# Kernel optimization log

Measured on AMD Instinct MI355X. Metric: run time of the kernel, lower is better.

Reference implementation:

```python
import jax, jax.numpy as jnp
import numpy as np

N, E, F, H = 20000, 320000, 128, 256   # nodes, edges, in-features, hidden
M, NQ = 4096, 2048                      # lsq rows, QP variables
LAMB_MAX = 2.0


def setup_inputs() -> dict:
    key = jax.random.key(0)
    ks = jax.random.split(key, 12)
    x = jax.random.normal(ks[0], (N, F), jnp.float32)
    edge_index = jax.random.randint(ks[1], (2, E), 0, N)
    A = jax.random.normal(ks[2], (M, NQ), jnp.float32) * 0.05
    b = jax.random.normal(ks[3], (M, 1), jnp.float32)
    feat_ids = jax.random.randint(ks[4], (NQ,), 0, N)
    x_prior = jax.random.uniform(ks[5], (NQ, 1), jnp.float32)
    lamb = jnp.ones((1,), jnp.float32)
    # ChebConv K=2 weights: one linear per Chebyshev order, plus bias
    W10 = jax.random.normal(ks[6], (F, H), jnp.float32) / np.sqrt(F)
    W11 = jax.random.normal(ks[7], (F, H), jnp.float32) / np.sqrt(F)
    b1 = jnp.zeros((H,), jnp.float32)
    W20 = jax.random.normal(ks[8], (H, 1), jnp.float32) / np.sqrt(H)
    W21 = jax.random.normal(ks[9], (H, 1), jnp.float32) / np.sqrt(H)
    b2 = jnp.zeros((1,), jnp.float32)
    return {"x": x, "edge_index": edge_index, "A": A, "b": b,
            "feat_ids": feat_ids, "x_prior": x_prior, "lamb": lamb,
            "W10": W10, "W11": W11, "b1": b1,
            "W20": W20, "W21": W21, "b2": b2}


def _cheb_conv(x, edge_index, W0, W1, bias, lam_max):
    """PyG ChebConv with K=2: out = x @ W0 + (2L/lam_max - I) x @ W1 + bias,
    L = I - D^{-1/2} A D^{-1/2}, via edge gather/scatter (no dense NxN)."""
    row, col = edge_index[0], edge_index[1]
    n = x.shape[0]
    deg = jax.ops.segment_sum(jnp.ones_like(row, dtype=x.dtype), row, num_segments=n)
    dinv = jnp.where(deg > 0, deg ** -0.5, 0.0)
    # normalized edge weight scaled by 2/lam_max, negated (off-diag of L_hat)
    w = -(2.0 / lam_max) * dinv[row] * dinv[col]              # [E]
    msg = jax.ops.segment_sum(w[:, None] * x[col], row, num_segments=n)
    Tx1 = msg + (2.0 / lam_max - 1.0) * x                      # diagonal of L_hat
    return x @ W0 + Tx1 @ W1 + bias


def reference(x, edge_index, A, b, feat_ids, x_prior, lamb,
              W10, W11, b1, W20, W21, b2):
    h = jax.nn.relu(_cheb_conv(x, edge_index, W10, W11, b1, LAMB_MAX))
    h = lamb[0] * jax.nn.relu(_cheb_conv(h, edge_index, W20, W21, b2, LAMB_MAX))
    hfold = h[feat_ids] + 1e-5                                 # [NQ, 1]
    q = hfold[:, 0]
    # QP: min 1/2 z^T Q z + p^T z with vacuous inequality (0*z <= 0.1) and no
    # equality constraints -> interior-point converges to unconstrained min.
    Q = A.T @ A + jnp.diag(q)                                  # [NQ, NQ]
    p = -(x_prior * hfold)[:, 0] - (b.T @ A)[0]                # [NQ]
    z = jnp.linalg.solve(Q, -p)                                # [NQ]
    return z[:, None]                                          # f.T -> [NQ, 1]
```

## Files before the change

### kernel.cpp

```cpp
#include <hip/hip_runtime.h>

#define N_NODES 20000
#define N_EDGES 320000
#define F_DIM   128
#define H_DIM   256
#define M_ROWS  4096
#define NQ      2048
#define NIT     18
#define MM_ROWS 20032

typedef __attribute__((ext_vector_type(8))) short short8;
typedef __attribute__((ext_vector_type(4))) float f32x4;


__device__ __forceinline__ float wred(float v) {
#pragma unroll
  for (int m = 32; m > 0; m >>= 1) v += __shfl_xor(v, m, 64);
  return v;
}

__device__ __forceinline__ float bred256(float v, float* lds) {
  v = wred(v);
  int w = threadIdx.x >> 6;
  if ((threadIdx.x & 63) == 0) lds[w] = v;
  __syncthreads();
  float tot = lds[0] + lds[1] + lds[2] + lds[3];
  __syncthreads();
  return tot;
}

__device__ __forceinline__ unsigned f2bf(float f) {
  unsigned u = __float_as_uint(f);
  unsigned r = u + 0x7fffu + ((u >> 16) & 1u);
  return r >> 16;
}
__device__ __forceinline__ float bflo(unsigned u) { return __uint_as_float(u << 16); }
__device__ __forceinline__ float bfhi(unsigned u) { return __uint_as_float(u & 0xffff0000u); }


__global__ __launch_bounds__(256) void k_deg(const int* __restrict__ ei, int* __restrict__ deg) {
  int e = blockIdx.x * 256 + threadIdx.x;
  if (e < N_EDGES) atomicAdd(&deg[ei[e]], 1);
}

__global__ __launch_bounds__(1024) void k_scan(const int* __restrict__ deg,
    int* __restrict__ rowstart, float* __restrict__ dinv) {
  __shared__ int part[1024];
  int t = threadIdx.x;
  const int chunk = (N_NODES + 1023) / 1024;
  int lo = t * chunk;
  int hi = lo + chunk; if (hi > N_NODES) hi = N_NODES;
  int s = 0;
  for (int i = lo; i < hi; ++i) {
    int d = deg[i];
    dinv[i] = d > 0 ? rsqrtf((float)d) : 0.f;
    s += d;
  }
  part[t] = s;
  __syncthreads();
  for (int off = 1; off < 1024; off <<= 1) {
    int v = part[t];
    int add = (t >= off) ? part[t - off] : 0;
    __syncthreads();
    part[t] = v + add;
    __syncthreads();
  }
  int base = (t > 0) ? part[t - 1] : 0;
  for (int i = lo; i < hi; ++i) { rowstart[i] = base; base += deg[i]; }
  if (t == 0) rowstart[N_NODES] = part[1023];
}

__global__ __launch_bounds__(256) void k_scatter(const int* __restrict__ ei,
    const int* __restrict__ rowstart, int* __restrict__ cursor,
    const float* __restrict__ dinv, int* __restrict__ cols, float* __restrict__ wvals) {
  int e = blockIdx.x * 256 + threadIdx.x;
  if (e >= N_EDGES) return;
  int r = ei[e];
  int c = ei[N_EDGES + e];
  int pos = rowstart[r] + atomicAdd(&cursor[r], 1);
  cols[pos] = c;
  wvals[pos] = -dinv[r] * dinv[c];
}

#define CONVX_BLKS (MM_ROWS * 16 / 256)

__global__ __launch_bounds__(256) void k_pack(const float* __restrict__ x,
    const float* __restrict__ W10, const float* __restrict__ W11,
    unsigned* __restrict__ xu, unsigned* __restrict__ Wtb) {
  int bx = blockIdx.x;
  if (bx < CONVX_BLKS) {
    int gid = bx * 256 + threadIdx.x;
    int row = gid >> 4;
    int q8 = gid & 15;
    uint4* xu4 = (uint4*)xu;
    if (row < N_NODES) {
      const float4* x4 = (const float4*)x;
      float4 a = x4[(size_t)row * 32 + q8 * 2];
      float4 b = x4[(size_t)row * 32 + q8 * 2 + 1];
      uint4 u;
      u.x = f2bf(a.x) | (f2bf(a.y) << 16);
      u.y = f2bf(a.z) | (f2bf(a.w) << 16);
      u.z = f2bf(b.x) | (f2bf(b.y) << 16);
      u.w = f2bf(b.z) | (f2bf(b.w) << 16);
      xu4[(size_t)row * 32 + q8] = u;
    } else {
      uint4 z = make_uint4(0, 0, 0, 0);
      xu4[(size_t)row * 32 + q8] = z;
      xu4[(size_t)row * 32 + 16 + q8] = z;
    }
  } else {
    int gid = (bx - CONVX_BLKS) * 256 + threadIdx.x;
    int n = gid >> 7;
    int u = gid & 127;
    int k0 = u * 2;
    float v0 = (k0 < 128) ? W10[(size_t)k0 * H_DIM + n]
                          : W11[(size_t)(k0 - 128) * H_DIM + n];
    float v1 = (k0 + 1 < 128) ? W10[(size_t)(k0 + 1) * H_DIM + n]
                              : W11[(size_t)(k0 - 127) * H_DIM + n];
    Wtb[(size_t)n * 128 + u] = f2bf(v0) | (f2bf(v1) << 16);
  }
}

__global__ __launch_bounds__(256) void k_msg1(const int* __restrict__ rowstart,
    const int* __restrict__ cols, const float* __restrict__ wvals,
    unsigned* __restrict__ xu) {
  int wid = (blockIdx.x * 256 + threadIdx.x) >> 6;
  int lane = threadIdx.x & 63;
  if (wid >= N_NODES) return;
  int s0 = rowstart[wid], s1 = rowstart[wid + 1];
  float2 acc = make_float2(0.f, 0.f);
  for (int e = s0; e < s1; ++e) {
    int c = cols[e];
    float w = wvals[e];
    unsigned u = xu[(size_t)c * 128 + lane];
    acc.x += w * bflo(u);
    acc.y += w * bfhi(u);
  }
  xu[(size_t)wid * 128 + 64 + lane] = f2bf(acc.x) | (f2bf(acc.y) << 16);
}

#define WS_ST 20

__global__ __launch_bounds__(256) void k_mm(const unsigned* __restrict__ xu,
    const unsigned* __restrict__ Wtb, const float* __restrict__ b1,
    const float* __restrict__ W20, const float* __restrict__ W21,
    float* __restrict__ t, float* __restrict__ s) {
  __shared__ unsigned Ws[2][256 * WS_ST];
  const int row0 = blockIdx.x * 64;
  const int tid = threadIdx.x;
  const int w = tid >> 6, lane = tid & 63;
  const int colb = w * 64;
  const int frow = lane & 15, fqo = (lane >> 4) * 4;
  const int c16 = lane & 15, q4 = lane >> 4;

  f32x4 acc[4][4];
#pragma unroll
  for (int a = 0; a < 4; ++a)
#pragma unroll
    for (int b = 0; b < 4; ++b) {
      acc[a][b][0] = 0.f; acc[a][b][1] = 0.f;
      acc[a][b][2] = 0.f; acc[a][b][3] = 0.f;
    }

  const uint4* Wtb4 = (const uint4*)Wtb;
  uint4 rw[4];
#pragma unroll
  for (int j = 0; j < 4; ++j) rw[j] = Wtb4[(size_t)tid * 32 + j];

  for (int kc = 0; kc < 8; ++kc) {
    const int b = kc & 1;
    unsigned* dst = Ws[b] + tid * WS_ST;
#pragma unroll
    for (int j = 0; j < 4; ++j) *(uint4*)(dst + j * 4) = rw[j];
    if (kc + 1 < 8) {
#pragma unroll
      for (int j = 0; j < 4; ++j) rw[j] = Wtb4[(size_t)tid * 32 + (kc + 1) * 4 + j];
    }
    __syncthreads();
    short8 af[4], bf[4];
#pragma unroll
    for (int a = 0; a < 4; ++a)
      af[a] = *(const short8*)(xu + (size_t)(row0 + a * 16 + frow) * 128 + kc * 16 + fqo);
#pragma unroll
    for (int n = 0; n < 4; ++n)
      bf[n] = *(const short8*)(Ws[b] + (colb + n * 16 + frow) * WS_ST + fqo);
#pragma unroll
    for (int a = 0; a < 4; ++a)
#pragma unroll
      for (int n = 0; n < 4; ++n)
        acc[a][n] = __builtin_amdgcn_mfma_f32_16x16x32_bf16(af[a], bf[n], acc[a][n], 0, 0, 0);
    __syncthreads();
  }

  float tp[4][4] = {}, sp[4][4] = {};
#pragma unroll
  for (int b2 = 0; b2 < 4; ++b2) {
    int gc = colb + b2 * 16 + c16;
    float w20 = W20[gc], w21 = W21[gc], bb = b1[gc];
#pragma unroll
    for (int a = 0; a < 4; ++a)
#pragma unroll
      for (int r = 0; r < 4; ++r) {
        float val = acc[a][b2][r] + bb;
        val = val > 0.f ? val : 0.f;
        tp[a][r] += val * w20;
        sp[a][r] += val * w21;
      }
  }
#pragma unroll
  for (int a = 0; a < 4; ++a)
#pragma unroll
    for (int r = 0; r < 4; ++r) {
#pragma unroll
      for (int m = 1; m < 16; m <<= 1) {
        tp[a][r] += __shfl_xor(tp[a][r], m, 64);
        sp[a][r] += __shfl_xor(sp[a][r], m, 64);
      }
    }
  if (c16 == 0) {
#pragma unroll
    for (int a = 0; a < 4; ++a)
#pragma unroll
      for (int r = 0; r < 4; ++r) {
        int gr = row0 + a * 16 + q4 * 4 + r;
        if (gr < N_NODES) {
          atomicAdd(&t[gr], tp[a][r]);
          atomicAdd(&s[gr], sp[a][r]);
        }
      }
  }
}


__global__ __launch_bounds__(256) void k_h2(const float* __restrict__ t,
    const float* __restrict__ s, const int* __restrict__ rowstart,
    const int* __restrict__ cols, const float* __restrict__ wvals,
    const float* __restrict__ lamb, const float* __restrict__ b2, float* __restrict__ h2) {
  int i = blockIdx.x * 256 + threadIdx.x;
  if (i >= N_NODES) return;
  float m = 0.f;
  int s0 = rowstart[i], s1 = rowstart[i + 1];
  for (int e = s0; e < s1; ++e) m += wvals[e] * s[cols[e]];
  float val = t[i] + m + b2[0];
  val = val > 0.f ? val : 0.f;
  h2[i] = lamb[0] * val;
}

__global__ __launch_bounds__(256) void k_prep(const float* __restrict__ A,
    const float* __restrict__ b, unsigned* __restrict__ Atu, float* __restrict__ btA_parts) {
  int jp = blockIdx.x * 256 + threadIdx.x;
  int k0 = blockIdx.y * 128;
  const float2* A2 = (const float2*)A;
  float acc0 = 0.f, acc1 = 0.f;
  for (int kk = 0; kk < 128; kk += 8) {
    float ax[8], ay[8];
#pragma unroll
    for (int i = 0; i < 8; ++i) {
      int k = k0 + kk + i;
      float2 a = A2[(size_t)k * 1024 + jp];
      float bk = b[k];
      acc0 += a.x * bk;
      acc1 += a.y * bk;
      ax[i] = a.x; ay[i] = a.y;
    }
    uint4 t0, t1;
    t0.x = f2bf(ax[0]) | (f2bf(ax[1]) << 16);
    t0.y = f2bf(ax[2]) | (f2bf(ax[3]) << 16);
    t0.z = f2bf(ax[4]) | (f2bf(ax[5]) << 16);
    t0.w = f2bf(ax[6]) | (f2bf(ax[7]) << 16);
    t1.x = f2bf(ay[0]) | (f2bf(ay[1]) << 16);
    t1.y = f2bf(ay[2]) | (f2bf(ay[3]) << 16);
    t1.z = f2bf(ay[4]) | (f2bf(ay[5]) << 16);
    t1.w = f2bf(ay[6]) | (f2bf(ay[7]) << 16);
    int uoff = (k0 + kk) >> 1;
    *(uint4*)(Atu + (size_t)(2 * jp) * 2048 + uoff) = t0;
    *(uint4*)(Atu + (size_t)(2 * jp + 1) * 2048 + uoff) = t1;
  }
  ((float2*)(btA_parts + (size_t)blockIdx.y * NQ))[jp] = make_float2(acc0, acc1);
}

__global__ __launch_bounds__(256) void k_qrhs(const float* __restrict__ h2,
    const int* __restrict__ feat_ids, const float* __restrict__ x_prior,
    const float* __restrict__ btA_parts, float* __restrict__ q, float* __restrict__ r) {
  int j = blockIdx.x * 256 + threadIdx.x;
  int f = feat_ids[j];
  float hf = h2[f] + 1e-5f;
  q[j] = hf;
  float bta = 0.f;
#pragma unroll
  for (int c = 0; c < 32; ++c) bta += btA_parts[(size_t)c * NQ + j];
  r[j] = x_prior[j] * hf + bta;
}

#define GR_ST 20

__global__ __launch_bounds__(512) void k_gram(const unsigned* __restrict__ Atu,
                                              float* __restrict__ Gp) {
  __shared__ unsigned shmem[10240];
  const int i0 = blockIdx.x * 128, j0 = blockIdx.y * 128;
  const int kz = blockIdx.z;
  const int tid = threadIdx.x;
  const int grp = tid >> 8;
  const int t8 = tid & 255;
  const int w = tid >> 6;
  const int wt = w & 3;
  const int lane = tid & 63;
  const int wr = (wt >> 1) * 64, wc = (wt & 1) * 64;
  const int srow = t8 >> 1, suo = (t8 & 1) * 8;
  const int frow = lane & 15, fqo = (lane >> 4) * 4;

  unsigned* shA = shmem + grp * 5120;
  unsigned* shB = shA + 2560;

  f32x4 acc[4][4];
#pragma unroll
  for (int a = 0; a < 4; ++a)
#pragma unroll
    for (int b = 0; b < 4; ++b) {
      acc[a][b][0] = 0.f; acc[a][b][1] = 0.f;
      acc[a][b][2] = 0.f; acc[a][b][3] = 0.f;
    }

  const unsigned* pa = Atu + (size_t)(i0 + srow) * 2048 + kz * 1024 + suo;
  const unsigned* pb = Atu + (size_t)(j0 + srow) * 2048 + kz * 1024 + suo;

  int ku = grp * 16;
  uint4 ra0 = *(const uint4*)(pa + ku);
  uint4 ra1 = *(const uint4*)(pa + ku + 4);
  uint4 rb0 = *(const uint4*)(pb + ku);
  uint4 rb1 = *(const uint4*)(pb + ku + 4);

  for (int si = 0; si < 32; ++si) {
    unsigned* as = shA + srow * GR_ST + suo;
    unsigned* bs = shB + srow * GR_ST + suo;
    *(uint4*)as = ra0; *(uint4*)(as + 4) = ra1;
    *(uint4*)bs = rb0; *(uint4*)(bs + 4) = rb1;
    if (si + 1 < 32) {
      ku = (si + 1) * 32 + grp * 16;
      ra0 = *(const uint4*)(pa + ku);
      ra1 = *(const uint4*)(pa + ku + 4);
      rb0 = *(const uint4*)(pb + ku);
      rb1 = *(const uint4*)(pb + ku + 4);
    }
    __syncthreads();
    short8 af[4], bf[4];
#pragma unroll
    for (int a = 0; a < 4; ++a)
      af[a] = *(const short8*)(shA + (wr + a * 16 + frow) * GR_ST + fqo);
#pragma unroll
    for (int b2 = 0; b2 < 4; ++b2)
      bf[b2] = *(const short8*)(shB + (wc + b2 * 16 + frow) * GR_ST + fqo);
#pragma unroll
    for (int a = 0; a < 4; ++a)
#pragma unroll
      for (int b2 = 0; b2 < 4; ++b2)
        acc[a][b2] = __builtin_amdgcn_mfma_f32_16x16x32_bf16(af[a], bf[b2], acc[a][b2], 0, 0, 0);
    __syncthreads();
  }

  const int q4 = lane >> 4, c16 = lane & 15;
  float* comb = (float*)shmem;
#pragma unroll
  for (int rnd = 0; rnd < 2; ++rnd) {
    if (grp == 1 && (wt >> 1) == rnd) {
      float* dst = comb + (wt & 1) * 4160;
#pragma unroll
      for (int a = 0; a < 4; ++a)
#pragma unroll
        for (int b2 = 0; b2 < 4; ++b2)
#pragma unroll
          for (int r = 0; r < 4; ++r)
            dst[(a * 16 + q4 * 4 + r) * 65 + b2 * 16 + c16] = acc[a][b2][r];
    }
    __syncthreads();
    if (grp == 0 && (wt >> 1) == rnd) {
      const float* src = comb + (wt & 1) * 4160;
#pragma unroll
      for (int a = 0; a < 4; ++a)
#pragma unroll
        for (int b2 = 0; b2 < 4; ++b2)
#pragma unroll
          for (int r = 0; r < 4; ++r)
            acc[a][b2][r] += src[(a * 16 + q4 * 4 + r) * 65 + b2 * 16 + c16];
    }
    __syncthreads();
  }

  if (grp == 0) {
    float* Gz = Gp + (size_t)kz * NQ * NQ;
#pragma unroll
    for (int a = 0; a < 4; ++a)
#pragma unroll
      for (int b2 = 0; b2 < 4; ++b2)
#pragma unroll
        for (int r = 0; r < 4; ++r) {
          int gr = i0 + wr + a * 16 + q4 * 4 + r;
          int gc = j0 + wc + b2 * 16 + c16;
          Gz[(size_t)gr * NQ + gc] = acc[a][b2][r];
        }
  }
}

__global__ __launch_bounds__(256) void k_gconv(const float* __restrict__ G0,
    const float* __restrict__ G1, const float* __restrict__ q,
    unsigned* __restrict__ Gb, float* __restrict__ qcorr) {
  int row = blockIdx.x;
  int tid = threadIdx.x;
  const float4* g04 = (const float4*)(G0 + (size_t)row * NQ);
  const float4* g14 = (const float4*)(G1 + (size_t)row * NQ);
  float4 a0 = g04[tid * 2], b0 = g04[tid * 2 + 1];
  float4 a1 = g14[tid * 2], b1 = g14[tid * 2 + 1];
  float v[8] = {a0.x + a1.x, a0.y + a1.y, a0.z + a1.z, a0.w + a1.w,
                b0.x + b1.x, b0.y + b1.y, b0.z + b1.z, b0.w + b1.w};
  bool diag = ((row >> 3) == tid);
  if (diag) v[row & 7] += q[row];
  uint4 u;
  u.x = f2bf(v[0]) | (f2bf(v[1]) << 16);
  u.y = f2bf(v[2]) | (f2bf(v[3]) << 16);
  u.z = f2bf(v[4]) | (f2bf(v[5]) << 16);
  u.w = f2bf(v[6]) | (f2bf(v[7]) << 16);
  ((uint4*)(Gb + (size_t)row * 1024))[tid] = u;
  if (diag) {
    float vd = v[row & 7];
    qcorr[row] = vd - __uint_as_float(f2bf(vd) << 16);
  }
}

__global__ __launch_bounds__(256) void k_cgG(int k, const unsigned* __restrict__ Gb,
    const float* __restrict__ qcorr,
    const float* __restrict__ r_old, float* __restrict__ r_new,
    const float* __restrict__ p_old, float* __restrict__ p_new,
    const float* __restrict__ Qp_in, float* __restrict__ Qp_out,
    float* __restrict__ xcg) {
  __shared__ float pshare[NQ];
  __shared__ float lds[4];
  const int tid = threadIdx.x, bid = blockIdx.x;
  const float4* r4 = (const float4*)r_old;
  float4 ra = r4[tid * 2], rb2 = r4[tid * 2 + 1];
  float pv[8];
  if (k == 0) {
    pv[0] = ra.x; pv[1] = ra.y; pv[2] = ra.z; pv[3] = ra.w;
    pv[4] = rb2.x; pv[5] = rb2.y; pv[6] = rb2.z; pv[7] = rb2.w;
    if (bid == 0) {
      ((float4*)p_new)[tid * 2] = ra;
      ((float4*)p_new)[tid * 2 + 1] = rb2;
    }
  } else {
    const float4* p4 = (const float4*)p_old;
    const float4* qp4 = (const float4*)Qp_in;
    float4 pa = p4[tid * 2], pb = p4[tid * 2 + 1];
    float4 qa = qp4[tid * 2], qb = qp4[tid * 2 + 1];
    float rr = ra.x * ra.x + ra.y * ra.y + ra.z * ra.z + ra.w * ra.w +
               rb2.x * rb2.x + rb2.y * rb2.y + rb2.z * rb2.z + rb2.w * rb2.w;
    float pap = pa.x * qa.x + pa.y * qa.y + pa.z * qa.z + pa.w * qa.w +
                pb.x * qb.x + pb.y * qb.y + pb.z * qb.z + pb.w * qb.w;
    rr = bred256(rr, lds);
    pap = bred256(pap, lds);
    float alpha = rr / pap;
    if (bid == 0) {
      float4* x4 = (float4*)xcg;
      float4 xa = x4[tid * 2], xb = x4[tid * 2 + 1];
      xa.x += alpha * pa.x; xa.y += alpha * pa.y;
      xa.z += alpha * pa.z; xa.w += alpha * pa.w;
      xb.x += alpha * pb.x; xb.y += alpha * pb.y;
      xb.z += alpha * pb.z; xb.w += alpha * pb.w;
      x4[tid * 2] = xa; x4[tid * 2 + 1] = xb;
    }
    ra.x -= alpha * qa.x; ra.y -= alpha * qa.y;
    ra.z -= alpha * qa.z; ra.w -= alpha * qa.w;
    rb2.x -= alpha * qb.x; rb2.y -= alpha * qb.y;
    rb2.z -= alpha * qb.z; rb2.w -= alpha * qb.w;
    float rrn = ra.x * ra.x + ra.y * ra.y + ra.z * ra.z + ra.w * ra.w +
                rb2.x * rb2.x + rb2.y * rb2.y + rb2.z * rb2.z + rb2.w * rb2.w;
    rrn = bred256(rrn, lds);
    float beta = rrn / rr;
    pv[0] = ra.x + beta * pa.x; pv[1] = ra.y + beta * pa.y;
    pv[2] = ra.z + beta * pa.z; pv[3] = ra.w + beta * pa.w;
    pv[4] = rb2.x + beta * pb.x; pv[5] = rb2.y + beta * pb.y;
    pv[6] = rb2.z + beta * pb.z; pv[7] = rb2.w + beta * pb.w;
    if (bid == 0) {
      ((float4*)r_new)[tid * 2] = ra;
      ((float4*)r_new)[tid * 2 + 1] = rb2;
      ((float4*)p_new)[tid * 2] = make_float4(pv[0], pv[1], pv[2], pv[3]);
      ((float4*)p_new)[tid * 2 + 1] = make_float4(pv[4], pv[5], pv[6], pv[7]);
    }
  }
  ((float4*)pshare)[tid * 2] = make_float4(pv[0], pv[1], pv[2], pv[3]);
  ((float4*)pshare)[tid * 2 + 1] = make_float4(pv[4], pv[5], pv[6], pv[7]);
  __syncthreads();
  const int w = tid >> 6, lane = tid & 63;
  const int row = bid * 4 + w;
  const uint4* Gr = (const uint4*)(Gb + (size_t)row * 1024);
  const float4* ps4 = (const float4*)pshare;
  float acc = 0.f;
#pragma unroll
  for (int c = 0; c < 4; ++c) {
    uint4 gv = Gr[c * 64 + lane];
    float4 pa = ps4[c * 128 + lane * 2];
    float4 pb = ps4[c * 128 + lane * 2 + 1];
    acc += bflo(gv.x) * pa.x + bfhi(gv.x) * pa.y;
    acc += bflo(gv.y) * pa.z + bfhi(gv.y) * pa.w;
    acc += bflo(gv.z) * pb.x + bfhi(gv.z) * pb.y;
    acc += bflo(gv.w) * pb.z + bfhi(gv.w) * pb.w;
  }
  acc = wred(acc);
  if (lane == 0) Qp_out[row] = acc + qcorr[row] * pshare[row];
}

__global__ __launch_bounds__(256) void k_cgfin(const float* __restrict__ r_last,
    const float* __restrict__ p_last, const float* __restrict__ Qp,
    const float* __restrict__ xcg, float* __restrict__ out) {
  const int tid = threadIdx.x;
  const int lane = tid & 63;
  const float4* r4 = (const float4*)r_last;
  const float4* p4 = (const float4*)p_last;
  const float4* q4 = (const float4*)Qp;
  float rr = 0.f, pap = 0.f;
#pragma unroll
  for (int c = 0; c < 4; ++c) {
#pragma unroll
    for (int hh = 0; hh < 2; ++hh) {
      float4 rv = r4[c * 128 + lane * 2 + hh];
      float4 pv = p4[c * 128 + lane * 2 + hh];
      float4 qv = q4[c * 128 + lane * 2 + hh];
      rr += rv.x * rv.x + rv.y * rv.y + rv.z * rv.z + rv.w * rv.w;
      pap += pv.x * qv.x + pv.y * qv.y + pv.z * qv.z + pv.w * qv.w;
    }
  }
  rr = wred(rr);
  pap = wred(pap);
  float alpha = rr / pap;
  const float4* x4 = (const float4*)xcg;
  float4* o4 = (float4*)out;
#pragma unroll
  for (int hh = 0; hh < 2; ++hh) {
    int i4 = tid * 2 + hh;
    float4 xv = x4[i4];
    float4 pv = p4[i4];
    xv.x += alpha * pv.x; xv.y += alpha * pv.y;
    xv.z += alpha * pv.z; xv.w += alpha * pv.w;
    o4[i4] = xv;
  }
}


extern "C" void kernel_launch(void* const* d_in, const int* in_sizes, int n_in,
                              void* d_out, int out_size, void* d_ws, size_t ws_size,
                              hipStream_t stream) {
  const float* x      = (const float*)d_in[0];
  const int*   ei     = (const int*)d_in[1];
  const float* A      = (const float*)d_in[2];
  const float* b      = (const float*)d_in[3];
  const int*   fids   = (const int*)d_in[4];
  const float* xprior = (const float*)d_in[5];
  const float* lamb   = (const float*)d_in[6];
  const float* W10    = (const float*)d_in[7];
  const float* W11    = (const float*)d_in[8];
  const float* b1     = (const float*)d_in[9];
  const float* W20    = (const float*)d_in[10];
  const float* W21    = (const float*)d_in[11];
  const float* b2     = (const float*)d_in[12];
  float* out = (float*)d_out;

  char* base = (char*)d_ws;
  size_t o = 0;
  auto alloc = [&](size_t bytes) { size_t r = o; o = (o + bytes + 255) & ~size_t(255); return r; };

  size_t off_deg    = alloc(N_NODES * 4);
  size_t off_cursor = alloc(N_NODES * 4);
  size_t off_xcg    = alloc(NQ * 4);
  size_t off_t      = alloc(N_NODES * 4);
  size_t off_s      = alloc(N_NODES * 4);
  size_t zero_end   = o;
  size_t off_rowst  = alloc((N_NODES + 1) * 4);
  size_t off_dinv   = alloc(N_NODES * 4);
  size_t off_h2     = alloc(N_NODES * 4);
  size_t off_q      = alloc(NQ * 4);
  size_t off_r0     = alloc(NQ * 4);
  size_t off_r1     = alloc(NQ * 4);
  size_t off_p0     = alloc(NQ * 4);
  size_t off_p1     = alloc(NQ * 4);
  size_t off_Qp0    = alloc(NQ * 4);
  size_t off_Qp1    = alloc(NQ * 4);
  size_t off_qcorr  = alloc(NQ * 4);
  size_t off_btAp   = alloc(32 * NQ * 4);
  size_t off_Wtb    = alloc(256 * 128 * 4);
  size_t sz_cols  = (size_t)N_EDGES * 4 + 256;
  size_t sz_wvals = (size_t)N_EDGES * 4 + 256;
  size_t sz_xmsg  = (size_t)MM_ROWS * 256 * 2;
  size_t union_gnn = sz_cols + sz_wvals + sz_xmsg;
  size_t union_at  = (size_t)M_ROWS * NQ * 2;
  size_t off_union = alloc(union_gnn > union_at ? union_gnn : union_at);
  size_t off_G0    = alloc((size_t)NQ * NQ * 4);
  size_t off_G1    = alloc((size_t)NQ * NQ * 4);
  if (o > ws_size) return;

  int*   deg      = (int*)(base + off_deg);
  int*   cursor   = (int*)(base + off_cursor);
  float* xcg      = (float*)(base + off_xcg);
  float* t        = (float*)(base + off_t);
  float* s        = (float*)(base + off_s);
  int*   rowstart = (int*)(base + off_rowst);
  float* dinv     = (float*)(base + off_dinv);
  float* h2       = (float*)(base + off_h2);
  float* q        = (float*)(base + off_q);
  float* rb[2]    = {(float*)(base + off_r0), (float*)(base + off_r1)};
  float* pg[2]    = {(float*)(base + off_p0), (float*)(base + off_p1)};
  float* Qpb[2]   = {(float*)(base + off_Qp0), (float*)(base + off_Qp1)};
  float* qcorr    = (float*)(base + off_qcorr);
  float* btA_parts = (float*)(base + off_btAp);
  unsigned* Wtb   = (unsigned*)(base + off_Wtb);
  int*   cols     = (int*)(base + off_union);
  float* wvals    = (float*)(base + off_union + sz_cols);
  unsigned* xmsgb = (unsigned*)(base + off_union + sz_cols + sz_wvals);
  unsigned* Atu   = (unsigned*)(base + off_union);
  unsigned* Gb    = (unsigned*)(base + off_union);
  float* G0       = (float*)(base + off_G0);
  float* G1       = (float*)(base + off_G1);

  hipMemsetAsync(d_ws, 0, zero_end, stream);

  k_deg<<<(N_EDGES + 255) / 256, 256, 0, stream>>>(ei, deg);
  k_scan<<<1, 1024, 0, stream>>>(deg, rowstart, dinv);
  k_scatter<<<(N_EDGES + 255) / 256, 256, 0, stream>>>(ei, rowstart, cursor, dinv, cols, wvals);

  k_pack<<<CONVX_BLKS + 128, 256, 0, stream>>>(x, W10, W11, xmsgb, Wtb);
  k_msg1<<<N_NODES / 4, 256, 0, stream>>>(rowstart, cols, wvals, xmsgb);
  k_mm<<<MM_ROWS / 64, 256, 0, stream>>>(xmsgb, Wtb, b1, W20, W21, t, s);
  k_h2<<<(N_NODES + 255) / 256, 256, 0, stream>>>(t, s, rowstart, cols, wvals, lamb, b2, h2);

  k_prep<<<dim3(4, 32), 256, 0, stream>>>(A, b, Atu, btA_parts);
  k_qrhs<<<NQ / 256, 256, 0, stream>>>(h2, fids, xprior, btA_parts, q, rb[0]);
  k_gram<<<dim3(16, 16, 2), 512, 0, stream>>>(Atu, G0);
  k_gconv<<<NQ, 256, 0, stream>>>(G0, G1, q, Gb, qcorr);

  k_cgG<<<512, 256, 0, stream>>>(0, Gb, qcorr, rb[0], rb[0], pg[0], pg[0],
                                 Qpb[1], Qpb[0], xcg);
  for (int k = 1; k < NIT; ++k) {
    k_cgG<<<512, 256, 0, stream>>>(k, Gb, qcorr, rb[(k - 1) & 1], rb[k & 1],
                                   pg[(k - 1) & 1], pg[k & 1],
                                   Qpb[(k - 1) & 1], Qpb[k & 1], xcg);
  }
  k_cgfin<<<1, 256, 0, stream>>>(rb[(NIT - 1) & 1], pg[(NIT - 1) & 1],
                                 Qpb[(NIT - 1) & 1], xcg, out);
}
```

Before: 412.9 us.

## Merge GNN and Gram stages into fewer multi-role kernels to cut launches

```diff
diff --git a/kernel.cpp b/kernel.cpp
--- a/kernel.cpp
+++ b/kernel.cpp
@@ -37,59 +37,19 @@
 __device__ __forceinline__ float bflo(unsigned u) { return __uint_as_float(u << 16); }
 __device__ __forceinline__ float bfhi(unsigned u) { return __uint_as_float(u & 0xffff0000u); }
 
-
-__global__ __launch_bounds__(256) void k_deg(const int* __restrict__ ei, int* __restrict__ deg) {
-  int e = blockIdx.x * 256 + threadIdx.x;
-  if (e < N_EDGES) atomicAdd(&deg[ei[e]], 1);
-}
-
-__global__ __launch_bounds__(1024) void k_scan(const int* __restrict__ deg,
-    int* __restrict__ rowstart, float* __restrict__ dinv) {
-  __shared__ int part[1024];
-  int t = threadIdx.x;
-  const int chunk = (N_NODES + 1023) / 1024;
-  int lo = t * chunk;
-  int hi = lo + chunk; if (hi > N_NODES) hi = N_NODES;
-  int s = 0;
-  for (int i = lo; i < hi; ++i) {
-    int d = deg[i];
-    dinv[i] = d > 0 ? rsqrtf((float)d) : 0.f;
-    s += d;
-  }
-  part[t] = s;
-  __syncthreads();
-  for (int off = 1; off < 1024; off <<= 1) {
-    int v = part[t];
-    int add = (t >= off) ? part[t - off] : 0;
-    __syncthreads();
-    part[t] = v + add;
-    __syncthreads();
-  }
-  int base = (t > 0) ? part[t - 1] : 0;
-  for (int i = lo; i < hi; ++i) { rowstart[i] = base; base += deg[i]; }
-  if (t == 0) rowstart[N_NODES] = part[1023];
-}
-
-__global__ __launch_bounds__(256) void k_scatter(const int* __restrict__ ei,
-    const int* __restrict__ rowstart, int* __restrict__ cursor,
-    const float* __restrict__ dinv, int* __restrict__ cols, float* __restrict__ wvals) {
-  int e = blockIdx.x * 256 + threadIdx.x;
-  if (e >= N_EDGES) return;
-  int r = ei[e];
-  int c = ei[N_EDGES + e];
-  int pos = rowstart[r] + atomicAdd(&cursor[r], 1);
-  cols[pos] = c;
-  wvals[pos] = -dinv[r] * dinv[c];
-}
-
-#define CONVX_BLKS (MM_ROWS * 16 / 256)
-
-__global__ __launch_bounds__(256) void k_pack(const float* __restrict__ x,
+#define DEG_BLKS ((N_EDGES + 255) / 256)
+#define PACK_X_BLKS (MM_ROWS * 16 / 256)
+
+__global__ __launch_bounds__(256) void k_init(const int* __restrict__ ei,
+    int* __restrict__ deg, const float* __restrict__ x,
     const float* __restrict__ W10, const float* __restrict__ W11,
     unsigned* __restrict__ xu, unsigned* __restrict__ Wtb) {
   int bx = blockIdx.x;
-  if (bx < CONVX_BLKS) {
-    int gid = bx * 256 + threadIdx.x;
+  if (bx < DEG_BLKS) {
+    int e = bx * 256 + threadIdx.x;
+    if (e < N_EDGES) atomicAdd(&deg[ei[e]], 1);
+  } else if (bx < DEG_BLKS + PACK_X_BLKS) {
+    int gid = (bx - DEG_BLKS) * 256 + threadIdx.x;
     int row = gid >> 4;
     int q8 = gid & 15;
     uint4* xu4 = (uint4*)xu;
@@ -109,7 +69,7 @@
       xu4[(size_t)row * 32 + 16 + q8] = z;
     }
   } else {
-    int gid = (bx - CONVX_BLKS) * 256 + threadIdx.x;
+    int gid = (bx - DEG_BLKS - PACK_X_BLKS) * 256 + threadIdx.x;
     int n = gid >> 7;
     int u = gid & 127;
     int k0 = u * 2;
@@ -121,22 +81,205 @@
   }
 }
 
-__global__ __launch_bounds__(256) void k_msg1(const int* __restrict__ rowstart,
+__global__ __launch_bounds__(1024) void k_scan(const int* __restrict__ deg,
+    int* __restrict__ rowstart, float* __restrict__ dinv) {
+  __shared__ int part[1024];
+  int t = threadIdx.x;
+  const int chunk = (N_NODES + 1023) / 1024;
+  int lo = t * chunk;
+  int hi = lo + chunk; if (hi > N_NODES) hi = N_NODES;
+  int s = 0;
+  for (int i = lo; i < hi; ++i) {
+    int d = deg[i];
+    dinv[i] = d > 0 ? rsqrtf((float)d) : 0.f;
+    s += d;
+  }
+  part[t] = s;
+  __syncthreads();
+  for (int off = 1; off < 1024; off <<= 1) {
+    int v = part[t];
+    int add = (t >= off) ? part[t - off] : 0;
+    __syncthreads();
+    part[t] = v + add;
+    __syncthreads();
+  }
+  int base = (t > 0) ? part[t - 1] : 0;
+  for (int i = lo; i < hi; ++i) { rowstart[i] = base; base += deg[i]; }
+  if (t == 0) rowstart[N_NODES] = part[1023];
+}
+
+__global__ __launch_bounds__(256) void k_build(const int* __restrict__ ei,
+    const int* __restrict__ rowstart, int* __restrict__ cursor,
+    const float* __restrict__ dinv, int* __restrict__ cols, float* __restrict__ wvals,
+    const float* __restrict__ A, const float* __restrict__ b,
+    unsigned* __restrict__ Atu, float* __restrict__ btA_parts) {
+  int bx = blockIdx.x;
+  if (bx < DEG_BLKS) {
+    int e = bx * 256 + threadIdx.x;
+    if (e >= N_EDGES) return;
+    int r = ei[e];
+    int c = ei[N_EDGES + e];
+    int pos = rowstart[r] + atomicAdd(&cursor[r], 1);
+    cols[pos] = c;
+    wvals[pos] = -dinv[r] * dinv[c];
+  } else {
+    int bp = bx - DEG_BLKS;
+    int jp = (bp & 3) * 256 + threadIdx.x;
+    int k0 = (bp >> 2) * 128;
+    const float2* A2 = (const float2*)A;
+    float acc0 = 0.f, acc1 = 0.f;
+    for (int kk = 0; kk < 128; kk += 8) {
+      float ax[8], ay[8];
+#pragma unroll
+      for (int i = 0; i < 8; ++i) {
+        int k = k0 + kk + i;
+        float2 a = A2[(size_t)k * 1024 + jp];
+        float bk = b[k];
+        acc0 += a.x * bk;
+        acc1 += a.y * bk;
+        ax[i] = a.x; ay[i] = a.y;
+      }
+      uint4 t0, t1;
+      t0.x = f2bf(ax[0]) | (f2bf(ax[1]) << 16);
+      t0.y = f2bf(ax[2]) | (f2bf(ax[3]) << 16);
+      t0.z = f2bf(ax[4]) | (f2bf(ax[5]) << 16);
+      t0.w = f2bf(ax[6]) | (f2bf(ax[7]) << 16);
+      t1.x = f2bf(ay[0]) | (f2bf(ay[1]) << 16);
+      t1.y = f2bf(ay[2]) | (f2bf(ay[3]) << 16);
+      t1.z = f2bf(ay[4]) | (f2bf(ay[5]) << 16);
+      t1.w = f2bf(ay[6]) | (f2bf(ay[7]) << 16);
+      int uoff = (k0 + kk) >> 1;
+      *(uint4*)(Atu + (size_t)(2 * jp) * 2048 + uoff) = t0;
+      *(uint4*)(Atu + (size_t)(2 * jp + 1) * 2048 + uoff) = t1;
+    }
+    ((float2*)(btA_parts + (size_t)(bp >> 2) * NQ))[jp] = make_float2(acc0, acc1);
+  }
+}
+
+#define GR_ST 20
+
+__global__ __launch_bounds__(512) void k_mega(const unsigned* __restrict__ Atu,
+    float* __restrict__ G, const int* __restrict__ rowstart,
     const int* __restrict__ cols, const float* __restrict__ wvals,
     unsigned* __restrict__ xu) {
-  int wid = (blockIdx.x * 256 + threadIdx.x) >> 6;
-  int lane = threadIdx.x & 63;
-  if (wid >= N_NODES) return;
-  int s0 = rowstart[wid], s1 = rowstart[wid + 1];
-  float2 acc = make_float2(0.f, 0.f);
-  for (int e = s0; e < s1; ++e) {
-    int c = cols[e];
-    float w = wvals[e];
-    unsigned u = xu[(size_t)c * 128 + lane];
-    acc.x += w * bflo(u);
-    acc.y += w * bfhi(u);
-  }
-  xu[(size_t)wid * 128 + 64 + lane] = f2bf(acc.x) | (f2bf(acc.y) << 16);
+  __shared__ unsigned shmem[10240];
+  const int blk = blockIdx.x;
+  if (blk >= 256) {
+    int row = (blk - 256) * 8 + (threadIdx.x >> 6);
+    int lane = threadIdx.x & 63;
+    if (row >= N_NODES) return;
+    int s0 = rowstart[row], s1 = rowstart[row + 1];
+    float2 acc = make_float2(0.f, 0.f);
+    for (int e = s0; e < s1; ++e) {
+      int c = cols[e];
+      float w = wvals[e];
+      unsigned u = xu[(size_t)c * 128 + lane];
+      acc.x += w * bflo(u);
+      acc.y += w * bfhi(u);
+    }
+    xu[(size_t)row * 128 + 64 + lane] = f2bf(acc.x) | (f2bf(acc.y) << 16);
+    return;
+  }
+  const int i0 = (blk >> 4) * 128, j0 = (blk & 15) * 128;
+  const int tid = threadIdx.x;
+  const int grp = tid >> 8;
+  const int t8 = tid & 255;
+  const int w = tid >> 6;
+  const int wt = w & 3;
+  const int lane = tid & 63;
+  const int wr = (wt >> 1) * 64, wc = (wt & 1) * 64;
+  const int srow = t8 >> 1, suo = (t8 & 1) * 8;
+  const int frow = lane & 15, fqo = (lane >> 4) * 4;
+
+  unsigned* shA = shmem + grp * 5120;
+  unsigned* shB = shA + 2560;
+
+  f32x4 acc[4][4];
+#pragma unroll
+  for (int a = 0; a < 4; ++a)
+#pragma unroll
+    for (int b = 0; b < 4; ++b) {
+      acc[a][b][0] = 0.f; acc[a][b][1] = 0.f;
+      acc[a][b][2] = 0.f; acc[a][b][3] = 0.f;
+    }
+
+  const unsigned* pa = Atu + (size_t)(i0 + srow) * 2048 + suo;
+  const unsigned* pb = Atu + (size_t)(j0 + srow) * 2048 + suo;
+
+  int ku = grp * 16;
+  uint4 ra0 = *(const uint4*)(pa + ku);
+  uint4 ra1 = *(const uint4*)(pa + ku + 4);
+  uint4 rb0 = *(const uint4*)(pb + ku);
+  uint4 rb1 = *(const uint4*)(pb + ku + 4);
+
+  for (int si = 0; si < 64; ++si) {
+    unsigned* as = shA + srow * GR_ST + suo;
+    unsigned* bs = shB + srow * GR_ST + suo;
+    *(uint4*)as = ra0; *(uint4*)(as + 4) = ra1;
+    *(uint4*)bs = rb0; *(uint4*)(bs + 4) = rb1;
+    if (si + 1 < 64) {
+      ku = (si + 1) * 32 + grp * 16;
+      ra0 = *(const uint4*)(pa + ku);
+      ra1 = *(const uint4*)(pa + ku + 4);
+      rb0 = *(const uint4*)(pb + ku);
+      rb1 = *(const uint4*)(pb + ku + 4);
+    }
+    __syncthreads();
+    short8 af[4], bf[4];
+#pragma unroll
+    for (int a = 0; a < 4; ++a)
+      af[a] = *(const short8*)(shA + (wr + a * 16 + frow) * GR_ST + fqo);
+#pragma unroll
+    for (int b2 = 0; b2 < 4; ++b2)
+      bf[b2] = *(const short8*)(shB + (wc + b2 * 16 + frow) * GR_ST + fqo);
+#pragma unroll
+    for (int a = 0; a < 4; ++a)
+#pragma unroll
+      for (int b2 = 0; b2 < 4; ++b2)
+        acc[a][b2] = __builtin_amdgcn_mfma_f32_16x16x32_bf16(af[a], bf[b2], acc[a][b2], 0, 0, 0);
+    __syncthreads();
+  }
+
+  const int q4 = lane >> 4, c16 = lane & 15;
+  float* comb = (float*)shmem;
+#pragma unroll
+  for (int rnd = 0; rnd < 2; ++rnd) {
+    if (grp == 1 && (wt >> 1) == rnd) {
+      float* dst = comb + (wt & 1) * 4160;
+#pragma unroll
+      for (int a = 0; a < 4; ++a)
+#pragma unroll
+        for (int b2 = 0; b2 < 4; ++b2)
+#pragma unroll
+          for (int r = 0; r < 4; ++r)
+            dst[(a * 16 + q4 * 4 + r) * 65 + b2 * 16 + c16] = acc[a][b2][r];
+    }
+    __syncthreads();
+    if (grp == 0 && (wt >> 1) == rnd) {
+      const float* src = comb + (wt & 1) * 4160;
+#pragma unroll
+      for (int a = 0; a < 4; ++a)
+#pragma unroll
+        for (int b2 = 0; b2 < 4; ++b2)
+#pragma unroll
+          for (int r = 0; r < 4; ++r)
+            acc[a][b2][r] += src[(a * 16 + q4 * 4 + r) * 65 + b2 * 16 + c16];
+    }
+    __syncthreads();
+  }
+
+  if (grp == 0) {
+#pragma unroll
+    for (int a = 0; a < 4; ++a)
+#pragma unroll
+      for (int b2 = 0; b2 < 4; ++b2)
+#pragma unroll
+        for (int r = 0; r < 4; ++r) {
+          int gr = i0 + wr + a * 16 + q4 * 4 + r;
+          int gc = j0 + wc + b2 * 16 + c16;
+          G[(size_t)gr * NQ + gc] = acc[a][b2][r];
+        }
+  }
 }
 
 #define WS_ST 20
@@ -246,174 +389,29 @@
   h2[i] = lamb[0] * val;
 }
 
-__global__ __launch_bounds__(256) void k_prep(const float* __restrict__ A,
-    const float* __restrict__ b, unsigned* __restrict__ Atu, float* __restrict__ btA_parts) {
-  int jp = blockIdx.x * 256 + threadIdx.x;
-  int k0 = blockIdx.y * 128;
-  const float2* A2 = (const float2*)A;
-  float acc0 = 0.f, acc1 = 0.f;
-  for (int kk = 0; kk < 128; kk += 8) {
-    float ax[8], ay[8];
-#pragma unroll
-    for (int i = 0; i < 8; ++i) {
-      int k = k0 + kk + i;
-      float2 a = A2[(size_t)k * 1024 + jp];
-      float bk = b[k];
-      acc0 += a.x * bk;
-      acc1 += a.y * bk;
-      ax[i] = a.x; ay[i] = a.y;
-    }
-    uint4 t0, t1;
-    t0.x = f2bf(ax[0]) | (f2bf(ax[1]) << 16);
-    t0.y = f2bf(ax[2]) | (f2bf(ax[3]) << 16);
-    t0.z = f2bf(ax[4]) | (f2bf(ax[5]) << 16);
-    t0.w = f2bf(ax[6]) | (f2bf(ax[7]) << 16);
-    t1.x = f2bf(ay[0]) | (f2bf(ay[1]) << 16);
-    t1.y = f2bf(ay[2]) | (f2bf(ay[3]) << 16);
-    t1.z = f2bf(ay[4]) | (f2bf(ay[5]) << 16);
-    t1.w = f2bf(ay[6]) | (f2bf(ay[7]) << 16);
-    int uoff = (k0 + kk) >> 1;
-    *(uint4*)(Atu + (size_t)(2 * jp) * 2048 + uoff) = t0;
-    *(uint4*)(Atu + (size_t)(2 * jp + 1) * 2048 + uoff) = t1;
-  }
-  ((float2*)(btA_parts + (size_t)blockIdx.y * NQ))[jp] = make_float2(acc0, acc1);
-}
-
-__global__ __launch_bounds__(256) void k_qrhs(const float* __restrict__ h2,
-    const int* __restrict__ feat_ids, const float* __restrict__ x_prior,
-    const float* __restrict__ btA_parts, float* __restrict__ q, float* __restrict__ r) {
-  int j = blockIdx.x * 256 + threadIdx.x;
-  int f = feat_ids[j];
-  float hf = h2[f] + 1e-5f;
-  q[j] = hf;
-  float bta = 0.f;
-#pragma unroll
-  for (int c = 0; c < 32; ++c) bta += btA_parts[(size_t)c * NQ + j];
-  r[j] = x_prior[j] * hf + bta;
-}
-
-#define GR_ST 20
-
-__global__ __launch_bounds__(512) void k_gram(const unsigned* __restrict__ Atu,
-                                              float* __restrict__ Gp) {
-  __shared__ unsigned shmem[10240];
-  const int i0 = blockIdx.x * 128, j0 = blockIdx.y * 128;
-  const int kz = blockIdx.z;
-  const int tid = threadIdx.x;
-  const int grp = tid >> 8;
-  const int t8 = tid & 255;
-  const int w = tid >> 6;
-  const int wt = w & 3;
-  const int lane = tid & 63;
-  const int wr = (wt >> 1) * 64, wc = (wt & 1) * 64;
-  const int srow = t8 >> 1, suo = (t8 & 1) * 8;
-  const int frow = lane & 15, fqo = (lane >> 4) * 4;
-
-  unsigned* shA = shmem + grp * 5120;
-  unsigned* shB = shA + 2560;
-
-  f32x4 acc[4][4];
-#pragma unroll
-  for (int a = 0; a < 4; ++a)
-#pragma unroll
-    for (int b = 0; b < 4; ++b) {
-      acc[a][b][0] = 0.f; acc[a][b][1] = 0.f;
-      acc[a][b][2] = 0.f; acc[a][b][3] = 0.f;
-    }
-
-  const unsigned* pa = Atu + (size_t)(i0 + srow) * 2048 + kz * 1024 + suo;
-  const unsigned* pb = Atu + (size_t)(j0 + srow) * 2048 + kz * 1024 + suo;
-
-  int ku = grp * 16;
-  uint4 ra0 = *(const uint4*)(pa + ku);
-  uint4 ra1 = *(const uint4*)(pa + ku + 4);
-  uint4 rb0 = *(const uint4*)(pb + ku);
-  uint4 rb1 = *(const uint4*)(pb + ku + 4);
-
-  for (int si = 0; si < 32; ++si) {
-    unsigned* as = shA + srow * GR_ST + suo;
-    unsigned* bs = shB + srow * GR_ST + suo;
-    *(uint4*)as = ra0; *(uint4*)(as + 4) = ra1;
-    *(uint4*)bs = rb0; *(uint4*)(bs + 4) = rb1;
-    if (si + 1 < 32) {
-      ku = (si + 1) * 32 + grp * 16;
-      ra0 = *(const uint4*)(pa + ku);
-      ra1 = *(const uint4*)(pa + ku + 4);
-      rb0 = *(const uint4*)(pb + ku);
-      rb1 = *(const uint4*)(pb + ku + 4);
-    }
-    __syncthreads();
-    short8 af[4], bf[4];
-#pragma unroll
-    for (int a = 0; a < 4; ++a)
-      af[a] = *(const short8*)(shA + (wr + a * 16 + frow) * GR_ST + fqo);
-#pragma unroll
-    for (int b2 = 0; b2 < 4; ++b2)
-      bf[b2] = *(const short8*)(shB + (wc + b2 * 16 + frow) * GR_ST + fqo);
-#pragma unroll
-    for (int a = 0; a < 4; ++a)
-#pragma unroll
-      for (int b2 = 0; b2 < 4; ++b2)
-        acc[a][b2] = __builtin_amdgcn_mfma_f32_16x16x32_bf16(af[a], bf[b2], acc[a][b2], 0, 0, 0);
-    __syncthreads();
-  }
-
-  const int q4 = lane >> 4, c16 = lane & 15;
-  float* comb = (float*)shmem;
-#pragma unroll
-  for (int rnd = 0; rnd < 2; ++rnd) {
-    if (grp == 1 && (wt >> 1) == rnd) {
-      float* dst = comb + (wt & 1) * 4160;
-#pragma unroll
-      for (int a = 0; a < 4; ++a)
-#pragma unroll
-        for (int b2 = 0; b2 < 4; ++b2)
-#pragma unroll
-          for (int r = 0; r < 4; ++r)
-            dst[(a * 16 + q4 * 4 + r) * 65 + b2 * 16 + c16] = acc[a][b2][r];
-    }
-    __syncthreads();
-    if (grp == 0 && (wt >> 1) == rnd) {
-      const float* src = comb + (wt & 1) * 4160;
-#pragma unroll
-      for (int a = 0; a < 4; ++a)
-#pragma unroll
-        for (int b2 = 0; b2 < 4; ++b2)
-#pragma unroll
-          for (int r = 0; r < 4; ++r)
-            acc[a][b2][r] += src[(a * 16 + q4 * 4 + r) * 65 + b2 * 16 + c16];
-    }
-    __syncthreads();
-  }
-
-  if (grp == 0) {
-    float* Gz = Gp + (size_t)kz * NQ * NQ;
-#pragma unroll
-    for (int a = 0; a < 4; ++a)
-#pragma unroll
-      for (int b2 = 0; b2 < 4; ++b2)
-#pragma unroll
-        for (int r = 0; r < 4; ++r) {
-          int gr = i0 + wr + a * 16 + q4 * 4 + r;
-          int gc = j0 + wc + b2 * 16 + c16;
-          Gz[(size_t)gr * NQ + gc] = acc[a][b2][r];
-        }
-  }
-}
-
-__global__ __launch_bounds__(256) void k_gconv(const float* __restrict__ G0,
-    const float* __restrict__ G1, const float* __restrict__ q,
-    unsigned* __restrict__ Gb, float* __restrict__ qcorr) {
-  int row = blockIdx.x;
-  int tid = threadIdx.x;
-  const float4* g04 = (const float4*)(G0 + (size_t)row * NQ);
-  const float4* g14 = (const float4*)(G1 + (size_t)row * NQ);
-  float4 a0 = g04[tid * 2], b0 = g04[tid * 2 + 1];
-  float4 a1 = g14[tid * 2], b1 = g14[tid * 2 + 1];
-  float v[8] = {a0.x + a1.x, a0.y + a1.y, a0.z + a1.z, a0.w + a1.w,
-                b0.x + b1.x, b0.y + b1.y, b0.z + b1.z, b0.w + b1.w};
+__global__ __launch_bounds__(256) void k_gq(const float* __restrict__ G,
+    const float* __restrict__ h2, const int* __restrict__ fids,
+    const float* __restrict__ xprior, const float* __restrict__ btA_parts,
+    unsigned* __restrict__ Gb, float* __restrict__ qcorr, float* __restrict__ r0) {
+  __shared__ float hfs;
+  const int row = blockIdx.x, tid = threadIdx.x;
+  if (tid < 32) {
+    float bta = btA_parts[(size_t)tid * NQ + row];
+#pragma unroll
+    for (int m = 16; m > 0; m >>= 1) bta += __shfl_xor(bta, m, 64);
+    if (tid == 0) {
+      float hf = h2[fids[row]] + 1e-5f;
+      hfs = hf;
+      r0[row] = xprior[row] * hf + bta;
+    }
+  }
+  __syncthreads();
+  float hf = hfs;
+  const float4* g4 = (const float4*)(G + (size_t)row * NQ);
+  float4 a0 = g4[tid * 2], b0 = g4[tid * 2 + 1];
+  float v[8] = {a0.x, a0.y, a0.z, a0.w, b0.x, b0.y, b0.z, b0.w};
   bool diag = ((row >> 3) == tid);
-  if (diag) v[row & 7] += q[row];
+  if (diag) v[row & 7] += hf;
   uint4 u;
   u.x = f2bf(v[0]) | (f2bf(v[1]) << 16);
   u.y = f2bf(v[2]) | (f2bf(v[3]) << 16);
@@ -575,7 +573,6 @@
   size_t off_rowst  = alloc((N_NODES + 1) * 4);
   size_t off_dinv   = alloc(N_NODES * 4);
   size_t off_h2     = alloc(N_NODES * 4);
-  size_t off_q      = alloc(NQ * 4);
   size_t off_r0     = alloc(NQ * 4);
   size_t off_r1     = alloc(NQ * 4);
   size_t off_p0     = alloc(NQ * 4);
@@ -588,11 +585,9 @@
   size_t sz_cols  = (size_t)N_EDGES * 4 + 256;
   size_t sz_wvals = (size_t)N_EDGES * 4 + 256;
   size_t sz_xmsg  = (size_t)MM_ROWS * 256 * 2;
-  size_t union_gnn = sz_cols + sz_wvals + sz_xmsg;
-  size_t union_at  = (size_t)M_ROWS * NQ * 2;
-  size_t off_union = alloc(union_gnn > union_at ? union_gnn : union_at);
-  size_t off_G0    = alloc((size_t)NQ * NQ * 4);
-  size_t off_G1    = alloc((size_t)NQ * NQ * 4);
+  size_t off_gnn  = alloc(sz_cols + sz_wvals + sz_xmsg);
+  size_t off_Atu  = alloc((size_t)M_ROWS * NQ * 2);
+  size_t off_G    = alloc((size_t)NQ * NQ * 4);
   if (o > ws_size) return;
 
   int*   deg      = (int*)(base + off_deg);
@@ -603,36 +598,29 @@
   int*   rowstart = (int*)(base + off_rowst);
   float* dinv     = (float*)(base + off_dinv);
   float* h2       = (float*)(base + off_h2);
-  float* q        = (float*)(base + off_q);
   float* rb[2]    = {(float*)(base + off_r0), (float*)(base + off_r1)};
   float* pg[2]    = {(float*)(base + off_p0), (float*)(base + off_p1)};
   float* Qpb[2]   = {(float*)(base + off_Qp0), (float*)(base + off_Qp1)};
   float* qcorr    = (float*)(base + off_qcorr);
   float* btA_parts = (float*)(base + off_btAp);
   unsigned* Wtb   = (unsigned*)(base + off_Wtb);
-  int*   cols     = (int*)(base + off_union);
-  float* wvals    = (float*)(base + off_union + sz_cols);
-  unsigned* xmsgb = (unsigned*)(base + off_union + sz_cols + sz_wvals);
-  unsigned* Atu   = (unsigned*)(base + off_union);
-  unsigned* Gb    = (unsigned*)(base + off_union);
-  float* G0       = (float*)(base + off_G0);
-  float* G1       = (float*)(base + off_G1);
+  int*   cols     = (int*)(base + off_gnn);
+  float* wvals    = (float*)(base + off_gnn + sz_cols);
+  unsigned* xmsgb = (unsigned*)(base + off_gnn + sz_cols + sz_wvals);
+  unsigned* Gb    = (unsigned*)(base + off_gnn);
+  unsigned* Atu   = (unsigned*)(base + off_Atu);
+  float* G        = (float*)(base + off_G);
 
   hipMemsetAsync(d_ws, 0, zero_end, stream);
 
-  k_deg<<<(N_EDGES + 255) / 256, 256, 0, stream>>>(ei, deg);
+  k_init<<<DEG_BLKS + PACK_X_BLKS + 128, 256, 0, stream>>>(ei, deg, x, W10, W11, xmsgb, Wtb);
   k_scan<<<1, 1024, 0, stream>>>(deg, rowstart, dinv);
-  k_scatter<<<(N_EDGES + 255) / 256, 256, 0, stream>>>(ei, rowstart, cursor, dinv, cols, wvals);
-
-  k_pack<<<CONVX_BLKS + 128, 256, 0, stream>>>(x, W10, W11, xmsgb, Wtb);
-  k_msg1<<<N_NODES / 4, 256, 0, stream>>>(rowstart, cols, wvals, xmsgb);
+  k_build<<<DEG_BLKS + 128, 256, 0, stream>>>(ei, rowstart, cursor, dinv, cols, wvals,
+                                              A, b, Atu, btA_parts);
+  k_mega<<<256 + (N_NODES + 7) / 8, 512, 0, stream>>>(Atu, G, rowstart, cols, wvals, xmsgb);
   k_mm<<<MM_ROWS / 64, 256, 0, stream>>>(xmsgb, Wtb, b1, W20, W21, t, s);
   k_h2<<<(N_NODES + 255) / 256, 256, 0, stream>>>(t, s, rowstart, cols, wvals, lamb, b2, h2);
-
-  k_prep<<<dim3(4, 32), 256, 0, stream>>>(A, b, Atu, btA_parts);
-  k_qrhs<<<NQ / 256, 256, 0, stream>>>(h2, fids, xprior, btA_parts, q, rb[0]);
-  k_gram<<<dim3(16, 16, 2), 512, 0, stream>>>(Atu, G0);
-  k_gconv<<<NQ, 256, 0, stream>>>(G0, G1, q, Gb, qcorr);
+  k_gq<<<NQ, 256, 0, stream>>>(G, h2, fids, xprior, btA_parts, Gb, qcorr, rb[0]);
 
   k_cgG<<<512, 256, 0, stream>>>(0, Gb, qcorr, rb[0], rb[0], pg[0], pg[0],
                                  Qpb[1], Qpb[0], xcg);
```

Measured after the change: 448.7 us. +8.7%, slower.
